# Kernel tuning notes

Hardware: AMD Instinct MI355X
Metric: run time of the kernel (lower is better)

Reference implementation:

```python
import jax, jax.numpy as jnp
import numpy as np
from jax import lax

N_FILTERS = 256
N_ITER = 20
N_HISTORY = 4
N_CLASSES = 100
BITS = 8            # n_bits_activ passed to Quan_layer
POOL_FREQ = 5
EPS = 1e-5


def quantize_ste(w, bits):
    # Uniform symmetric quantization to `bits` with straight-through estimator.
    n = 2.0 ** (bits - 1) - 1.0
    s = jnp.max(jnp.abs(w)) / n
    q = jnp.round(w / s) * s
    return w + lax.stop_gradient(q - w)


def max_pool2(x):
    return lax.reduce_window(x, -jnp.inf, lax.max, (1, 1, 2, 2), (1, 1, 2, 2), 'VALID')


def setup_inputs() -> dict:
    key = jax.random.key(0)
    ks = jax.random.split(key, 5)
    x = jax.random.normal(ks[0], (16, 3, 64, 64), jnp.float32)
    conv_w = jax.random.normal(ks[1], (N_FILTERS, N_FILTERS, 3, 3), jnp.float32) / np.sqrt(9.0 * N_FILTERS).astype(np.float32)
    alpha = jnp.zeros((N_ITER, N_HISTORY + 1), jnp.float32)
    alpha = alpha.at[:, 0].set(0.1).at[:, 1].set(0.9)
    alpha = alpha + 0.01 * jax.random.normal(ks[2], (N_ITER, N_HISTORY + 1), jnp.float32)
    bn_gamma = jnp.ones((N_ITER, N_FILTERS), jnp.float32)
    bn_beta = jnp.zeros((N_ITER, N_FILTERS), jnp.float32)
    out_w = jax.random.normal(ks[3], (N_CLASSES, N_FILTERS), jnp.float32) / np.sqrt(float(N_FILTERS)).astype(np.float32)
    out_b = jnp.zeros((N_CLASSES,), jnp.float32)
    return {'x': x, 'conv_w': conv_w, 'alpha': alpha, 'bn_gamma': bn_gamma,
            'bn_beta': bn_beta, 'out_w': out_w, 'out_b': out_b}


def reference(x, conv_w, alpha, bn_gamma, bn_beta, out_w, out_b):
    pool_at = [t % POOL_FREQ == POOL_FREQ - 1 for t in range(N_ITER)]
    c_in = x.shape[1]
    # zero-pad channels up to n_filters (F.pad on dim 1)
    x = jnp.pad(x, ((0, 0), (0, N_FILTERS - c_in), (0, 0), (0, 0)))
    hist = [None] * (N_HISTORY - 1) + [x]
    wq = quantize_ste(conv_w, BITS)  # shared quantized conv weight
    for t in range(N_ITER):
        a = lax.conv_general_dilated(hist[-1], wq, (1, 1), ((1, 1), (1, 1)),
                                     dimension_numbers=('NCHW', 'OIHW', 'NCHW'))
        a = jax.nn.relu(a)
        a = alpha[t, 0] * a
        for i, h in enumerate(hist):
            if h is not None:
                a = a + alpha[t, i + 1] * h
        # BatchNorm2d (training-mode batch stats, biased variance)
        mean = jnp.mean(a, axis=(0, 2, 3), keepdims=True)
        var = jnp.var(a, axis=(0, 2, 3), keepdims=True)
        a = (a - mean) / jnp.sqrt(var + EPS)
        a = a * bn_gamma[t][None, :, None, None] + bn_beta[t][None, :, None, None]
        # faithful shift: hist[0] is never overwritten (stays None)
        hist = [hist[0]] + hist[2:] + [a]
        if pool_at[t]:
            hist = [None if h is None else max_pool2(h) for h in hist]
    out = jnp.max(hist[-1], axis=(2, 3))  # adaptive_max_pool2d -> (1,1)
    return out @ out_w.T + out_b
```

## Files before the change

### kernel.cpp

```cpp
#include <hip/hip_runtime.h>
#include <hip/hip_fp16.h>
#include <cstddef>
#include <cstdint>


#define NB 16
#define NIT 20

typedef _Float16 half8 __attribute__((ext_vector_type(8)));
typedef _Float16 half4v __attribute__((ext_vector_type(4)));
typedef float floatx4 __attribute__((ext_vector_type(4)));

__device__ __forceinline__ void gl_lds16(const void* g, void* l) {
  __builtin_amdgcn_global_load_lds(
      (const __attribute__((address_space(1))) unsigned int*)g,
      (__attribute__((address_space(3))) unsigned int*)l, 16, 0, 0);
}

__global__ void wmax_part_kernel(const float* __restrict__ w, float* __restrict__ part, int n) {
  float m = 0.f;
  for (int i = blockIdx.x * blockDim.x + threadIdx.x; i < n; i += gridDim.x * blockDim.x)
    m = fmaxf(m, fabsf(w[i]));
  #pragma unroll
  for (int o = 32; o > 0; o >>= 1) m = fmaxf(m, __shfl_down(m, o));
  __shared__ float sm[4];
  int wid = threadIdx.x >> 6, lane = threadIdx.x & 63;
  if (lane == 0) sm[wid] = m;
  __syncthreads();
  if (threadIdx.x == 0) part[blockIdx.x] = fmaxf(fmaxf(sm[0], sm[1]), fmaxf(sm[2], sm[3]));
}

__global__ void wmax_final_kernel(const float* __restrict__ part, float* __restrict__ sout) {
  float m = part[threadIdx.x];
  #pragma unroll
  for (int o = 32; o > 0; o >>= 1) m = fmaxf(m, __shfl_down(m, o));
  __shared__ float sm[4];
  int wid = threadIdx.x >> 6, lane = threadIdx.x & 63;
  if (lane == 0) sm[wid] = m;
  __syncthreads();
  if (threadIdx.x == 0) sout[0] = fmaxf(fmaxf(sm[0], sm[1]), fmaxf(sm[2], sm[3])) / 127.f;
}

__global__ void quant_kernel(const float* __restrict__ w, const float* __restrict__ sptr,
                             _Float16* __restrict__ wqr, int nw) {
  int d = blockIdx.x * 256 + threadIdx.x;
  if (d >= nw) return;
  int frag = d >> 9;
  int e = d & 511;
  int l = e >> 3, j = e & 7;
  int tap = frag >> 7;
  int rem = frag & 127;
  int cog = rem >> 3, chk = rem & 7;
  int co = cog * 16 + (l & 15);
  int ci = chk * 32 + (l >> 4) * 8 + j;
  float s = sptr[0];
  float q = rintf(w[((size_t)co * 256 + ci) * 9 + tap] / s) * s;
  wqr[d] = (_Float16)q;
}

__global__ void pad_kernel(const float* __restrict__ x, _Float16* __restrict__ out) {
  int idx = blockIdx.x * 256 + threadIdx.x;
  int c = idx & 255;
  int pos = idx >> 8;
  int hw = pos & 4095;
  int n = pos >> 12;
  float v = 0.f;
  if (c < 3) v = x[(n * 3 + c) * 4096 + hw];
  out[idx] = (_Float16)v;
}

template <int S, int WR>
__global__ __launch_bounds__(512, 2) void conv_mfma_big(
    const _Float16* __restrict__ in, const _Float16* __restrict__ wqr,
    const float* __restrict__ alpha, int t,
    const _Float16* h1, const _Float16* __restrict__ h2,
    const _Float16* __restrict__ h3, _Float16* pre,
    const _Float16* __restrict__ zpage,
    float* __restrict__ psum, float* __restrict__ psum2) {
  constexpr int R = 8 * WR;
  constexpr int LW = S + 2;
  constexpr int PIX = (R + 2) * LW;
  constexpr int XS = PIX * 4;
  constexpr int XS_PAD = ((XS + 63) / 64) * 64;
  constexpr int WS = 36 * 64;

  __shared__ half8 xl[2][XS_PAD];
  __shared__ half8 wl[2][WS];

  const int tid = threadIdx.x;
  const int lane = tid & 63;
  const int wn = tid >> 6;
  const int l16 = lane & 15;
  const int kg = lane >> 4;

  constexpr int BPI = S / R;
  const int n = blockIdx.x / BPI;
  const int rb = blockIdx.x % BPI;
  const int cob = blockIdx.y * 64;

  const _Float16* img = in + (size_t)n * S * S * 256;

  floatx4 acc[4][4];
  #pragma unroll
  for (int f = 0; f < 4; ++f)
    #pragma unroll
    for (int g = 0; g < 4; ++g)
      acc[f][g] = (floatx4){0.f, 0.f, 0.f, 0.f};

  auto stage = [&](int buf, int c) {
    const _Float16* cbase = img + c * 32;
    for (int sb = wn * 64; sb < XS_PAD; sb += 512) {
      int slot = sb + lane;
      const void* g = (const void*)zpage;
      if (slot < XS) {
        int pix = slot >> 2;
        int cig = (slot & 3) ^ ((pix >> 1) & 3);
        int hp = pix / LW, wp = pix - hp * LW;
        int h = rb * R + hp - 1, w = wp - 1;
        if ((unsigned)h < (unsigned)S && (unsigned)w < (unsigned)S)
          g = (const void*)(cbase + (size_t)(h * S + w) * 256 + cig * 8);
      }
      gl_lds16(g, (void*)&xl[buf][sb]);
    }
    for (int fb = wn; fb < 36; fb += 8) {
      int tap = fb >> 2, cf = fb & 3;
      const _Float16* g = wqr +
          ((((size_t)tap * 16 + blockIdx.y * 4 + cf) * 8 + c) << 9) + lane * 8;
      gl_lds16((const void*)g, (void*)&wl[buf][fb * 64]);
    }
  };

  auto compute = [&](int buf) {
    #pragma unroll
    for (int dh = -1; dh <= 1; ++dh) {
      #pragma unroll
      for (int dw = -1; dw <= 1; ++dw) {
        const int tap = (dh + 1) * 3 + (dw + 1);
        half8 af[4];
        #pragma unroll
        for (int f = 0; f < 4; ++f)
          af[f] = wl[buf][(tap * 4 + f) * 64 + lane];
        half8 bf[4];
        #pragma unroll
        for (int g = 0; g < 4; ++g) {
          int lp = wn * 64 + g * 16 + l16;
          int r = lp / S, cc = lp - r * S;
          int xp = (r + 1 + dh) * LW + (cc + 1 + dw);
          bf[g] = xl[buf][xp * 4 + (kg ^ ((xp >> 1) & 3))];
        }
        #pragma unroll
        for (int f = 0; f < 4; ++f)
          #pragma unroll
          for (int g = 0; g < 4; ++g)
            acc[f][g] = __builtin_amdgcn_mfma_f32_16x16x32_f16(af[f], bf[g], acc[f][g], 0, 0, 0);
      }
    }
  };

  stage(0, 0);
  __syncthreads();
  for (int c = 0; c < 8; ++c) {
    if (c < 7) stage((c + 1) & 1, c + 1);
    compute(c & 1);
    __syncthreads();
  }

  const float a0 = alpha[t * 5 + 0];
  const float a1 = alpha[t * 5 + 2];
  const float a2 = alpha[t * 5 + 3];
  const float a3 = alpha[t * 5 + 4];
  float ss[4][4], s2[4][4];
  #pragma unroll
  for (int f = 0; f < 4; ++f)
    #pragma unroll
    for (int r = 0; r < 4; ++r) { ss[f][r] = 0.f; s2[f][r] = 0.f; }

  const size_t pixbase = (size_t)n * S * S + (size_t)rb * R * S;
  #pragma unroll
  for (int f = 0; f < 4; ++f) {
    const int co = cob + f * 16 + kg * 4;
    #pragma unroll
    for (int g = 0; g < 4; ++g) {
      int lp = wn * 64 + g * 16 + l16;
      size_t idx = (pixbase + lp) * 256 + co;
      half4v v3 = *(const half4v*)(h3 + idx);
      half4v v1 = {}, v2 = {};
      if (h1) v1 = *(const half4v*)(h1 + idx);
      if (h2) v2 = *(const half4v*)(h2 + idx);
      half4v o;
      #pragma unroll
      for (int r = 0; r < 4; ++r) {
        float pv = a0 * fmaxf(acc[f][g][r], 0.f) + a3 * (float)v3[r];
        if (h1) pv += a1 * (float)v1[r];
        if (h2) pv += a2 * (float)v2[r];
        o[r] = (_Float16)pv;
        ss[f][r] += pv;
        s2[f][r] += pv * pv;
      }
      *(half4v*)(pre + idx) = o;
    }
  }

  float* sred = (float*)(&wl[0][0]);
  #pragma unroll
  for (int f = 0; f < 4; ++f)
    #pragma unroll
    for (int r = 0; r < 4; ++r) {
      float a = ss[f][r], b = s2[f][r];
      #pragma unroll
      for (int m = 1; m < 16; m <<= 1) {
        a += __shfl_xor(a, m);
        b += __shfl_xor(b, m);
      }
      if (l16 == 0) {
        sred[wn * 64 + f * 16 + kg * 4 + r] = a;
        sred[512 + wn * 64 + f * 16 + kg * 4 + r] = b;
      }
    }
  __syncthreads();
  if (tid < 64) {
    float a = 0.f, b = 0.f;
    #pragma unroll
    for (int w = 0; w < 8; ++w) {
      a += sred[w * 64 + tid];
      b += sred[512 + w * 64 + tid];
    }
    psum[(size_t)blockIdx.x * 256 + cob + tid] = a;
    psum2[(size_t)blockIdx.x * 256 + cob + tid] = b;
  }
}

template <int S, int R>
__global__ __launch_bounds__(512, 2) void conv_mfma_sm(
    const _Float16* __restrict__ in, const _Float16* __restrict__ wqr,
    const float* __restrict__ alpha, int t,
    const _Float16* h1, const _Float16* __restrict__ h2,
    const _Float16* __restrict__ h3, _Float16* pre,
    const _Float16* __restrict__ zpage,
    float* __restrict__ psum, float* __restrict__ psum2) {
  constexpr int LW = S + 2;
  constexpr int PIX = (R + 2) * LW;
  constexpr int XS = PIX * 4;
  constexpr int XS_PAD = ((XS + 63) / 64) * 64;
  constexpr int WS = 36 * 64;
  constexpr int PIXB = R * S;
  constexpr int G = PIXB / 64;

  __shared__ half8 xl[2][XS_PAD];
  __shared__ half8 wl[2][WS];
  __shared__ float sred[8][4][2][4];
  __shared__ float sredq[8][4][2][4];

  const int tid = threadIdx.x;
  const int lane = tid & 63;
  const int wid = tid >> 6;
  const int l16 = lane & 15;
  const int kg = lane >> 4;
  const int wm = wid >> 2;
  const int wn = wid & 3;

  constexpr int BPI = S / R;
  const int n = blockIdx.x / BPI;
  const int rb = blockIdx.x % BPI;
  const int cob = blockIdx.y * 64;

  const _Float16* img = in + (size_t)n * S * S * 256;

  floatx4 acc[2][G];
  #pragma unroll
  for (int f = 0; f < 2; ++f)
    #pragma unroll
    for (int g = 0; g < G; ++g)
      acc[f][g] = (floatx4){0.f, 0.f, 0.f, 0.f};

  auto stage = [&](int buf, int c) {
    const _Float16* cbase = img + c * 32;
    for (int sb = wid * 64; sb < XS_PAD; sb += 512) {
      int slot = sb + lane;
      const void* g = (const void*)zpage;
      if (slot < XS) {
        int pix = slot >> 2;
        int cig = (slot & 3) ^ ((pix >> 1) & 3);
        int hp = pix / LW, wp = pix - hp * LW;
        int h = rb * R + hp - 1, w = wp - 1;
        if ((unsigned)h < (unsigned)S && (unsigned)w < (unsigned)S)
          g = (const void*)(cbase + (size_t)(h * S + w) * 256 + cig * 8);
      }
      gl_lds16(g, (void*)&xl[buf][sb]);
    }
    for (int fb = wid; fb < 36; fb += 8) {
      int tap = fb >> 2, cogl = fb & 3;
      const _Float16* g = wqr +
          ((((size_t)tap * 16 + blockIdx.y * 4 + cogl) * 8 + c) << 9) + lane * 8;
      gl_lds16((const void*)g, (void*)&wl[buf][fb * 64]);
    }
  };

  auto compute = [&](int buf) {
    #pragma unroll
    for (int dh = -1; dh <= 1; ++dh) {
      #pragma unroll
      for (int dw = -1; dw <= 1; ++dw) {
        const int tap = (dh + 1) * 3 + (dw + 1);
        half8 af[2];
        #pragma unroll
        for (int f = 0; f < 2; ++f)
          af[f] = wl[buf][(tap * 4 + wm * 2 + f) * 64 + lane];
        half8 bf[G];
        #pragma unroll
        for (int g = 0; g < G; ++g) {
          int p = wn * (PIXB / 4) + g * 16 + l16;
          int r = p / S, cc = p - r * S;
          int lp = (r + 1 + dh) * LW + (cc + 1 + dw);
          bf[g] = xl[buf][lp * 4 + (kg ^ ((lp >> 1) & 3))];
        }
        #pragma unroll
        for (int f = 0; f < 2; ++f)
          #pragma unroll
          for (int g = 0; g < G; ++g)
            acc[f][g] = __builtin_amdgcn_mfma_f32_16x16x32_f16(af[f], bf[g], acc[f][g], 0, 0, 0);
      }
    }
  };

  stage(0, 0);
  __syncthreads();
  for (int c = 0; c < 8; ++c) {
    if (c < 7) stage((c + 1) & 1, c + 1);
    compute(c & 1);
    __syncthreads();
  }

  const float a0 = alpha[t * 5 + 0];
  const float a1 = alpha[t * 5 + 2];
  const float a2 = alpha[t * 5 + 3];
  const float a3 = alpha[t * 5 + 4];
  float ss[2][4], sq[2][4];
  #pragma unroll
  for (int f = 0; f < 2; ++f)
    #pragma unroll
    for (int r = 0; r < 4; ++r) { ss[f][r] = 0.f; sq[f][r] = 0.f; }

  const size_t pix0 = (size_t)n * S * S + (size_t)rb * PIXB;
  #pragma unroll
  for (int f = 0; f < 2; ++f) {
    const int co = cob + wm * 32 + f * 16 + kg * 4;
    #pragma unroll
    for (int g = 0; g < G; ++g) {
      int p = wn * (PIXB / 4) + g * 16 + l16;
      size_t idx = (pix0 + p) * 256 + co;
      half4v v3 = *(const half4v*)(h3 + idx);
      half4v v1 = {}, v2 = {};
      if (h1) v1 = *(const half4v*)(h1 + idx);
      if (h2) v2 = *(const half4v*)(h2 + idx);
      half4v o;
      #pragma unroll
      for (int r = 0; r < 4; ++r) {
        float pv = a0 * fmaxf(acc[f][g][r], 0.f) + a3 * (float)v3[r];
        if (h1) pv += a1 * (float)v1[r];
        if (h2) pv += a2 * (float)v2[r];
        o[r] = (_Float16)pv;
        ss[f][r] += pv;
        sq[f][r] += pv * pv;
      }
      *(half4v*)(pre + idx) = o;
    }
  }

  #pragma unroll
  for (int f = 0; f < 2; ++f)
    #pragma unroll
    for (int r = 0; r < 4; ++r) {
      float a = ss[f][r], b = sq[f][r];
      #pragma unroll
      for (int m = 1; m < 16; m <<= 1) {
        a += __shfl_xor(a, m);
        b += __shfl_xor(b, m);
      }
      if (l16 == 0) { sred[wid][kg][f][r] = a; sredq[wid][kg][f][r] = b; }
    }
  __syncthreads();
  if (tid < 64) {
    int ch = tid;
    int wmm = ch >> 5, ff = (ch >> 4) & 1, kk = (ch >> 2) & 3, rr = ch & 3;
    float a = 0.f, b = 0.f;
    #pragma unroll
    for (int w = 0; w < 4; ++w) {
      a += sred[wmm * 4 + w][kk][ff][rr];
      b += sredq[wmm * 4 + w][kk][ff][rr];
    }
    psum[(size_t)blockIdx.x * 256 + cob + ch] = a;
    psum2[(size_t)blockIdx.x * 256 + cob + ch] = b;
  }
}

__global__ void stats_final_kernel(const float* __restrict__ psum, const float* __restrict__ psum2,
                                   const float* __restrict__ gamma, const float* __restrict__ beta,
                                   int t, float M, int nblk,
                                   float* __restrict__ scale, float* __restrict__ shift) {
  int c = blockIdx.x;
  float s = 0.f, s2 = 0.f;
  for (int b = threadIdx.x; b < nblk; b += 64) {
    s += psum[(size_t)b * 256 + c];
    s2 += psum2[(size_t)b * 256 + c];
  }
  #pragma unroll
  for (int o = 32; o > 0; o >>= 1) {
    s += __shfl_down(s, o);
    s2 += __shfl_down(s2, o);
  }
  if (threadIdx.x == 0) {
    float mean = s / M;
    float var = s2 / M - mean * mean;
    float sc = gamma[t * 256 + c] * rsqrtf(var + 1e-5f);
    scale[c] = sc;
    shift[c] = beta[t * 256 + c] - mean * sc;
  }
}

__global__ void apply_kernel(_Float16* __restrict__ x, const float* __restrict__ scale,
                             const float* __restrict__ shift, int n8) {
  int i = blockIdx.x * 256 + threadIdx.x;
  if (i >= n8) return;
  half8 v = *(half8*)(x + (size_t)i * 8);
  int c0 = (i * 8) & 255;
  half8 o;
  #pragma unroll
  for (int j = 0; j < 8; ++j) o[j] = (_Float16)((float)v[j] * scale[c0 + j] + shift[c0 + j]);
  *(half8*)(x + (size_t)i * 8) = o;
}

__global__ void pool3_kernel(const _Float16* __restrict__ s0, const _Float16* __restrict__ s1,
                             const _Float16* __restrict__ s2,
                             _Float16* __restrict__ d0, _Float16* __restrict__ d1,
                             _Float16* __restrict__ d2,
                             const float* __restrict__ scale, const float* __restrict__ shift,
                             int So, int total8) {
  int i = blockIdx.x * 256 + threadIdx.x;
  if (i >= total8) return;
  int z = blockIdx.y;
  const _Float16* in = (z == 0) ? s0 : (z == 1) ? s1 : s2;
  _Float16* out = (z == 0) ? d0 : (z == 1) ? d1 : d2;
  int c0 = (i & 31) * 8;
  int pix = i >> 5;
  int wo = pix % So;
  int t1 = pix / So;
  int ho = t1 % So;
  int n = t1 / So;
  int Si = So * 2;
  size_t b00 = ((size_t)(n * Si * Si) + (2 * ho) * Si + 2 * wo) * 256 + c0;
  half8 v00 = *(const half8*)(in + b00);
  half8 v01 = *(const half8*)(in + b00 + 256);
  half8 v10 = *(const half8*)(in + b00 + (size_t)Si * 256);
  half8 v11 = *(const half8*)(in + b00 + (size_t)Si * 256 + 256);
  half8 o;
  if (z == 2) {
    #pragma unroll
    for (int j = 0; j < 8; ++j) {
      float sc = scale[c0 + j], sh = shift[c0 + j];
      float a = (float)v00[j] * sc + sh;
      float b = (float)v01[j] * sc + sh;
      float c = (float)v10[j] * sc + sh;
      float d = (float)v11[j] * sc + sh;
      o[j] = (_Float16)fmaxf(fmaxf(a, b), fmaxf(c, d));
    }
  } else {
    #pragma unroll
    for (int j = 0; j < 8; ++j) {
      float m = fmaxf(fmaxf((float)v00[j], (float)v01[j]),
                      fmaxf((float)v10[j], (float)v11[j]));
      o[j] = (_Float16)m;
    }
  }
  *(half8*)(out + (size_t)pix * 256 + c0) = o;
}

__global__ void amax_kernel(const _Float16* __restrict__ x, float* __restrict__ vec) {
  int i = blockIdx.x * blockDim.x + threadIdx.x;
  if (i >= NB * 256) return;
  int n = i >> 8, c = i & 255;
  float m = -1e30f;
  for (int p = 0; p < 16; ++p)
    m = fmaxf(m, (float)x[((size_t)(n * 16 + p)) * 256 + c]);
  vec[i] = m;
}

__global__ void linear_kernel(const float* __restrict__ vec, const float* __restrict__ W,
                              const float* __restrict__ b, float* __restrict__ out) {
  int n = blockIdx.x, j = threadIdx.x;
  if (j >= 100) return;
  float s = b[j];
  const float* v = vec + n * 256;
  const float* w = W + j * 256;
  for (int c = 0; c < 256; ++c) s += v[c] * w[c];
  out[n * 100 + j] = s;
}

extern "C" void kernel_launch(void* const* d_in, const int* in_sizes, int n_in,
                              void* d_out, int out_size, void* d_ws, size_t ws_size,
                              hipStream_t stream) {
  const float* x        = (const float*)d_in[0];
  const float* conv_w   = (const float*)d_in[1];
  const float* alpha    = (const float*)d_in[2];
  const float* bn_gamma = (const float*)d_in[3];
  const float* bn_beta  = (const float*)d_in[4];
  const float* out_w    = (const float*)d_in[5];
  const float* out_b    = (const float*)d_in[6];
  float* out = (float*)d_out;

  char* ws = (char*)d_ws;
  size_t off = 0;
  auto alloc = [&](size_t bytes) -> void* {
    void* p = (void*)(ws + off);
    off = (off + bytes + 255) & ~(size_t)255;
    return p;
  };
  const size_t SLAB = (size_t)NB * 4096 * 256 * 2;
  char* slab[4];
  size_t slabsz[4];
  for (int i = 0; i < 3; ++i) { slab[i] = (char*)alloc(SLAB); slabsz[i] = SLAB; }
  slab[3] = (char*)alloc(3 * (SLAB / 4)); slabsz[3] = 3 * (SLAB / 4);
  _Float16* wqr  = (_Float16*)alloc((size_t)9 * 256 * 256 * 2);
  float* wpart = (float*)alloc(256 * 4);
  float* sq    = (float*)alloc(256);
  float* psum  = (float*)alloc(256 * 256 * 4);
  float* psum2 = (float*)alloc(256 * 256 * 4);
  float* scale = (float*)alloc(256 * 4);
  float* shift = (float*)alloc(256 * 4);
  float* vec   = (float*)alloc((size_t)NB * 256 * 4);
  _Float16* zpage = (_Float16*)alloc(256);
  (void)ws_size;

  const int NW = 256 * 256 * 9;

  hipMemsetAsync(zpage, 0, 256, stream);

  hipLaunchKernelGGL(wmax_part_kernel, dim3(256), dim3(256), 0, stream, conv_w, wpart, NW);
  hipLaunchKernelGGL(wmax_final_kernel, dim3(1), dim3(256), 0, stream, wpart, sq);
  hipLaunchKernelGGL(quant_kernel, dim3((NW + 255) / 256), dim3(256), 0, stream, conv_w, sq, wqr, NW);

  hipLaunchKernelGGL(pad_kernel, dim3((NB * 4096 * 256) / 256), dim3(256), 0, stream,
                     x, (_Float16*)slab[0]);

  auto contains = [&](int k, char* p) -> bool {
    return p && p >= slab[k] && p < slab[k] + slabsz[k];
  };

  char *p1 = nullptr, *p2 = nullptr, *p3 = slab[0];
  int S = 64;
  for (int t = 0; t < NIT; ++t) {
    char* dst;
    if (p1) {
      dst = p1;
    } else {
      dst = nullptr;
      for (int k = 0; k < 3; ++k)
        if (!contains(k, p2) && !contains(k, p3)) { dst = slab[k]; break; }
    }
    const _Float16* h1 = (const _Float16*)p1;
    const _Float16* h2 = (const _Float16*)p2;
    const _Float16* h3 = (const _Float16*)p3;
    _Float16* pre = (_Float16*)dst;

    int nblk;
    dim3 block(512);
    switch (S) {
      case 64: {
        dim3 grid(NB * 8, 4);  nblk = NB * 8;
        hipLaunchKernelGGL((conv_mfma_big<64, 1>), grid, block, 0, stream,
                           h3, wqr, alpha, t, h1, h2, h3, pre, zpage, psum, psum2);
        break;
      }
      case 32: {
        dim3 grid(NB * 2, 4);  nblk = NB * 2;
        hipLaunchKernelGGL((conv_mfma_big<32, 2>), grid, block, 0, stream,
                           h3, wqr, alpha, t, h1, h2, h3, pre, zpage, psum, psum2);
        break;
      }
      case 16: {
        dim3 grid(NB * 4, 4);  nblk = NB * 4;
        hipLaunchKernelGGL((conv_mfma_sm<16, 4>), grid, block, 0, stream,
                           h3, wqr, alpha, t, h1, h2, h3, pre, zpage, psum, psum2);
        break;
      }
      default: {
        dim3 grid(NB * 1, 4);  nblk = NB * 1;
        hipLaunchKernelGGL((conv_mfma_sm<8, 8>), grid, block, 0, stream,
                           h3, wqr, alpha, t, h1, h2, h3, pre, zpage, psum, psum2);
        break;
      }
    }

    int npix = NB * S * S;
    hipLaunchKernelGGL(stats_final_kernel, dim3(256), dim3(64), 0, stream,
                       psum, psum2, bn_gamma, bn_beta, t, (float)npix, nblk, scale, shift);

    if (t % 5 != 4) {
      int n8 = npix * 32;
      hipLaunchKernelGGL(apply_kernel, dim3((n8 + 255) / 256), dim3(256), 0, stream,
                         pre, scale, shift, n8);
      p1 = p2; p2 = p3; p3 = dst;
    } else {
      char* q1 = p2;
      char* q2 = p3;
      char* q3 = dst;
      int So = S / 2;
      size_t qbytes = (size_t)NB * So * So * 256 * 2;
      char* fs = nullptr;
      for (int k = 0; k < 4; ++k)
        if (!contains(k, q1) && !contains(k, q2) && !contains(k, q3)) { fs = slab[k]; break; }
      int total8 = NB * So * So * 32;
      dim3 pg((total8 + 255) / 256, 3);
      hipLaunchKernelGGL(pool3_kernel, pg, dim3(256), 0, stream,
                         (const _Float16*)q1, (const _Float16*)q2, (const _Float16*)q3,
                         (_Float16*)fs, (_Float16*)(fs + qbytes), (_Float16*)(fs + 2 * qbytes),
                         scale, shift, So, total8);
      p1 = fs; p2 = fs + qbytes; p3 = fs + 2 * qbytes;
      S = So;
    }
  }

  hipLaunchKernelGGL(amax_kernel, dim3(16), dim3(256), 0, stream, (const _Float16*)p3, vec);
  hipLaunchKernelGGL(linear_kernel, dim3(NB), dim3(128), 0, stream, vec, out_w, out_b, out);
}
```

Baseline: 1.155 ms.

## Restructure large-image conv into per-tap weight staging with 2D wave tiling

The 64x64 and 32x32 conv kernels are replaced by a templated kernel that stages weights one tap at a time instead of all nine taps per channel chunk. The weight double buffer shrinks, and the k-loop runs over 72 chunk-tap steps. Waves are arranged in a 2D grid over output channels and pixels, allowing 128-channel tiles with fewer image rows per block, and pixel coordinates are precomputed. The aim is smaller LDS use, higher occupancy and more input-tile reuse across channels, at the cost of a barrier on every tap step.

```diff
diff --git a/kernel.cpp b/kernel.cpp
--- a/kernel.cpp
+++ b/kernel.cpp
@@ -69,36 +69,45 @@
   out[idx] = (_Float16)v;
 }
 
-template <int S, int WR>
-__global__ __launch_bounds__(512, 2) void conv_mfma_big(
+template <int S, int R, int CO_B, int NWAVES, int MINW>
+__global__ __launch_bounds__(NWAVES * 64, MINW) void conv_mfma_v5(
     const _Float16* __restrict__ in, const _Float16* __restrict__ wqr,
     const float* __restrict__ alpha, int t,
     const _Float16* h1, const _Float16* __restrict__ h2,
     const _Float16* __restrict__ h3, _Float16* pre,
     const _Float16* __restrict__ zpage,
     float* __restrict__ psum, float* __restrict__ psum2) {
-  constexpr int R = 8 * WR;
+  constexpr int NT = NWAVES * 64;
   constexpr int LW = S + 2;
-  constexpr int PIX = (R + 2) * LW;
-  constexpr int XS = PIX * 4;
+  constexpr int XS = (R + 2) * LW * 4;
   constexpr int XS_PAD = ((XS + 63) / 64) * 64;
-  constexpr int WS = 36 * 64;
+  constexpr int FRAGS = CO_B / 16;
 
   __shared__ half8 xl[2][XS_PAD];
-  __shared__ half8 wl[2][WS];
+  __shared__ half8 wl[2][FRAGS * 64];
 
   const int tid = threadIdx.x;
   const int lane = tid & 63;
-  const int wn = tid >> 6;
+  const int wid = tid >> 6;
   const int l16 = lane & 15;
   const int kg = lane >> 4;
+  const int wm = wid >> 2;
+  const int wn = wid & 3;
 
   constexpr int BPI = S / R;
   const int n = blockIdx.x / BPI;
   const int rb = blockIdx.x % BPI;
-  const int cob = blockIdx.y * 64;
+  const int cob = blockIdx.y * CO_B;
 
   const _Float16* img = in + (size_t)n * S * S * 256;
+
+  int rg[4], cg[4];
+  #pragma unroll
+  for (int g = 0; g < 4; ++g) {
+    int lp = wn * 64 + g * 16 + l16;
+    rg[g] = lp / S;
+    cg[g] = lp - rg[g] * S;
+  }
 
   floatx4 acc[4][4];
   #pragma unroll
@@ -107,9 +116,9 @@
     for (int g = 0; g < 4; ++g)
       acc[f][g] = (floatx4){0.f, 0.f, 0.f, 0.f};
 
-  auto stage = [&](int buf, int c) {
+  auto stageX = [&](int buf, int c) {
     const _Float16* cbase = img + c * 32;
-    for (int sb = wn * 64; sb < XS_PAD; sb += 512) {
+    for (int sb = wid * 64; sb < XS_PAD; sb += NT) {
       int slot = sb + lane;
       const void* g = (const void*)zpage;
       if (slot < XS) {
@@ -122,46 +131,46 @@
       }
       gl_lds16(g, (void*)&xl[buf][sb]);
     }
-    for (int fb = wn; fb < 36; fb += 8) {
-      int tap = fb >> 2, cf = fb & 3;
-      const _Float16* g = wqr +
-          ((((size_t)tap * 16 + blockIdx.y * 4 + cf) * 8 + c) << 9) + lane * 8;
-      gl_lds16((const void*)g, (void*)&wl[buf][fb * 64]);
-    }
   };
-
-  auto compute = [&](int buf) {
-    #pragma unroll
-    for (int dh = -1; dh <= 1; ++dh) {
+  auto stageW = [&](int buf, int c, int tap) {
+    const _Float16* g = wqr +
+        ((((size_t)tap * 16 + blockIdx.y * FRAGS + wid) * 8 + c) << 9) + lane * 8;
+    gl_lds16((const void*)g, (void*)&wl[buf][wid * 64]);
+  };
+
+  stageX(0, 0);
+  stageW(0, 0, 0);
+  __syncthreads();
+
+  for (int s = 0; s < 72; ++s) {
+    const int c = s / 9;
+    const int tap = s - c * 9;
+    if (s < 71) {
+      const int s2 = s + 1;
+      const int c2 = s2 / 9;
+      stageW(s2 & 1, c2, s2 - c2 * 9);
+    }
+    if (tap == 0 && c < 7) stageX((c + 1) & 1, c + 1);
+
+    const int dh = tap / 3 - 1;
+    const int dw = tap - (tap / 3) * 3 - 1;
+    const int wbuf = s & 1, xbuf = c & 1;
+
+    half8 af[4];
+    #pragma unroll
+    for (int f = 0; f < 4; ++f)
+      af[f] = wl[wbuf][(wm * 4 + f) * 64 + lane];
+    half8 bf[4];
+    #pragma unroll
+    for (int g = 0; g < 4; ++g) {
+      int xp = (rg[g] + 1 + dh) * LW + (cg[g] + 1 + dw);
+      bf[g] = xl[xbuf][xp * 4 + (kg ^ ((xp >> 1) & 3))];
+    }
+    #pragma unroll
+    for (int f = 0; f < 4; ++f)
       #pragma unroll
-      for (int dw = -1; dw <= 1; ++dw) {
-        const int tap = (dh + 1) * 3 + (dw + 1);
-        half8 af[4];
-        #pragma unroll
-        for (int f = 0; f < 4; ++f)
-          af[f] = wl[buf][(tap * 4 + f) * 64 + lane];
-        half8 bf[4];
-        #pragma unroll
-        for (int g = 0; g < 4; ++g) {
-          int lp = wn * 64 + g * 16 + l16;
-          int r = lp / S, cc = lp - r * S;
-          int xp = (r + 1 + dh) * LW + (cc + 1 + dw);
-          bf[g] = xl[buf][xp * 4 + (kg ^ ((xp >> 1) & 3))];
-        }
-        #pragma unroll
-        for (int f = 0; f < 4; ++f)
-          #pragma unroll
-          for (int g = 0; g < 4; ++g)
-            acc[f][g] = __builtin_amdgcn_mfma_f32_16x16x32_f16(af[f], bf[g], acc[f][g], 0, 0, 0);
-      }
-    }
-  };
-
-  stage(0, 0);
-  __syncthreads();
-  for (int c = 0; c < 8; ++c) {
-    if (c < 7) stage((c + 1) & 1, c + 1);
-    compute(c & 1);
+      for (int g = 0; g < 4; ++g)
+        acc[f][g] = __builtin_amdgcn_mfma_f32_16x16x32_f16(af[f], bf[g], acc[f][g], 0, 0, 0);
     __syncthreads();
   }
 
@@ -169,16 +178,16 @@
   const float a1 = alpha[t * 5 + 2];
   const float a2 = alpha[t * 5 + 3];
   const float a3 = alpha[t * 5 + 4];
-  float ss[4][4], s2[4][4];
+  float ss[4][4], s2v[4][4];
   #pragma unroll
   for (int f = 0; f < 4; ++f)
     #pragma unroll
-    for (int r = 0; r < 4; ++r) { ss[f][r] = 0.f; s2[f][r] = 0.f; }
+    for (int r = 0; r < 4; ++r) { ss[f][r] = 0.f; s2v[f][r] = 0.f; }
 
   const size_t pixbase = (size_t)n * S * S + (size_t)rb * R * S;
   #pragma unroll
   for (int f = 0; f < 4; ++f) {
-    const int co = cob + f * 16 + kg * 4;
+    const int co = cob + wm * 64 + f * 16 + kg * 4;
     #pragma unroll
     for (int g = 0; g < 4; ++g) {
       int lp = wn * 64 + g * 16 + l16;
@@ -195,7 +204,7 @@
         if (h2) pv += a2 * (float)v2[r];
         o[r] = (_Float16)pv;
         ss[f][r] += pv;
-        s2[f][r] += pv * pv;
+        s2v[f][r] += pv * pv;
       }
       *(half4v*)(pre + idx) = o;
     }
@@ -206,24 +215,26 @@
   for (int f = 0; f < 4; ++f)
     #pragma unroll
     for (int r = 0; r < 4; ++r) {
-      float a = ss[f][r], b = s2[f][r];
+      float a = ss[f][r], b = s2v[f][r];
       #pragma unroll
       for (int m = 1; m < 16; m <<= 1) {
         a += __shfl_xor(a, m);
         b += __shfl_xor(b, m);
       }
       if (l16 == 0) {
-        sred[wn * 64 + f * 16 + kg * 4 + r] = a;
-        sred[512 + wn * 64 + f * 16 + kg * 4 + r] = b;
+        sred[wid * 64 + f * 16 + kg * 4 + r] = a;
+        sred[NWAVES * 64 + wid * 64 + f * 16 + kg * 4 + r] = b;
       }
     }
   __syncthreads();
-  if (tid < 64) {
+  if (tid < CO_B) {
+    int half = tid >> 6;
+    int ch = tid & 63;
     float a = 0.f, b = 0.f;
     #pragma unroll
-    for (int w = 0; w < 8; ++w) {
-      a += sred[w * 64 + tid];
-      b += sred[512 + w * 64 + tid];
+    for (int w = 0; w < 4; ++w) {
+      a += sred[(half * 4 + w) * 64 + ch];
+      b += sred[NWAVES * 64 + (half * 4 + w) * 64 + ch];
     }
     psum[(size_t)blockIdx.x * 256 + cob + tid] = a;
     psum2[(size_t)blockIdx.x * 256 + cob + tid] = b;
@@ -563,29 +574,28 @@
     _Float16* pre = (_Float16*)dst;
 
     int nblk;
-    dim3 block(512);
     switch (S) {
       case 64: {
-        dim3 grid(NB * 8, 4);  nblk = NB * 8;
-        hipLaunchKernelGGL((conv_mfma_big<64, 1>), grid, block, 0, stream,
+        dim3 grid(NB * 16, 2);  nblk = NB * 16;
+        hipLaunchKernelGGL((conv_mfma_v5<64, 4, 128, 8, 4>), grid, dim3(512), 0, stream,
                            h3, wqr, alpha, t, h1, h2, h3, pre, zpage, psum, psum2);
         break;
       }
       case 32: {
-        dim3 grid(NB * 2, 4);  nblk = NB * 2;
-        hipLaunchKernelGGL((conv_mfma_big<32, 2>), grid, block, 0, stream,
+        dim3 grid(NB * 4, 4);  nblk = NB * 4;
+        hipLaunchKernelGGL((conv_mfma_v5<32, 8, 64, 4, 2>), grid, dim3(256), 0, stream,
                            h3, wqr, alpha, t, h1, h2, h3, pre, zpage, psum, psum2);
         break;
       }
       case 16: {
         dim3 grid(NB * 4, 4);  nblk = NB * 4;
-        hipLaunchKernelGGL((conv_mfma_sm<16, 4>), grid, block, 0, stream,
+        hipLaunchKernelGGL((conv_mfma_sm<16, 4>), grid, dim3(512), 0, stream,
                            h3, wqr, alpha, t, h1, h2, h3, pre, zpage, psum, psum2);
         break;
       }
       default: {
         dim3 grid(NB * 1, 4);  nblk = NB * 1;
-        hipLaunchKernelGGL((conv_mfma_sm<8, 8>), grid, block, 0, stream,
+        hipLaunchKernelGGL((conv_mfma_sm<8, 8>), grid, dim3(512), 0, stream,
                            h3, wqr, alpha, t, h1, h2, h3, pre, zpage, psum, psum2);
         break;
       }
```

Result: slower. 1.203 ms (+4.2%).
